# Performance work log

Hardware: AMD Instinct MI355X
Metric: run time of the kernel (lower is better)

The kernel has to match this reference:

```python
import jax, jax.numpy as jnp
import numpy as np

N = 100_000        # nodes
E = 3_200_000      # edges (avg degree 32)
H = 20             # hidden_channels (forced by forward body)
EH = 64            # edge_hidden_dim
EOUT = 10          # edge_output_dim (forced: 10 + EOUT == H)
THRESHOLD = 10.0


def setup_inputs() -> dict:
    key = jax.random.key(0)
    ks = jax.random.split(key, 12)
    x = jax.random.normal(ks[0], (N, 2, H), dtype=jnp.float32)
    edge_index = jax.random.randint(ks[1], (2, E), 0, N, dtype=jnp.int32)
    # distances must be in (0, threshold]
    edge_attr = jax.random.uniform(ks[2], (E, 1), dtype=jnp.float32, minval=1e-3, maxval=THRESHOLD)
    # module parameters (match torch init distributions: uniform[0,1))
    a = jax.random.uniform(ks[3], (1,), dtype=jnp.float32)
    b = jax.random.uniform(ks[4], (1,), dtype=jnp.float32) + 1.0
    gamma1 = jax.random.uniform(ks[5], (H, H), dtype=jnp.float32)
    gamma2 = jax.random.uniform(ks[6], (H, H), dtype=jnp.float32)
    bias = jax.random.uniform(ks[7], (H,), dtype=jnp.float32)
    # EdgeFeatureMLP2 params: Linear(1->EH), Linear(EH->EOUT)
    W1 = jax.random.normal(ks[8], (1, EH), dtype=jnp.float32)
    b1 = jax.random.normal(ks[9], (EH,), dtype=jnp.float32) * 0.1
    W2 = jax.random.normal(ks[10], (EH, EOUT), dtype=jnp.float32) / np.sqrt(EH)
    b2 = jax.random.normal(ks[11], (EOUT,), dtype=jnp.float32) * 0.1
    return dict(x=x, edge_index=edge_index, edge_attr=edge_attr, a=a, b=b,
                gamma1=gamma1, gamma2=gamma2, bias=bias, W1=W1, b1=b1, W2=W2, b2=b2)


def reference(x, edge_index, edge_attr, a, b, gamma1, gamma2, bias, W1, b1, W2, b2):
    src, dst = edge_index[0], edge_index[1]
    # edge MLP: Linear -> ReLU -> Linear -> ReLU
    h = jax.nn.relu(edge_attr @ W1 + b1)                    # [E, EH]
    mlp_out = jax.nn.relu(h @ W2 + b2)                      # [E, EOUT]
    # one-hot distance bucket: int(d / (threshold/10)), clipped to 9
    idx = jnp.minimum((edge_attr[:, 0] / (THRESHOLD / 10.0)).astype(jnp.int32), 9)
    one_hot = jax.nn.one_hot(idx, 10, dtype=edge_attr.dtype)  # [E, 10]
    comb = jnp.concatenate([one_hot, mlp_out], axis=1)      # [E, 20]
    # w_tilde: per-edge features normalized by the sum over all edges from the source node
    sum_w = jax.ops.segment_sum(comb, src, num_segments=N)  # [N, 20]
    sw = sum_w[src]                                         # [E, 20]
    nz = sw != 0
    w_tilde = jnp.where(nz, comb / jnp.where(nz, sw, 1.0), 0.01)
    # rho weighting: |a*h_j - (1-a)*h_j'|^b, elementwise over the 20-dim slot-0 features
    rho = jnp.abs(a * x[src, 0] - (1.0 - a) * x[dst, 0]) ** b  # [E, 20]
    sum_feat = jax.ops.segment_sum(rho * w_tilde, src, num_segments=N)  # [N, 20]
    # node update: relu(gamma1 @ x_j + gamma2 @ sum_feat_j + bias)
    out0 = jax.nn.relu(x[:, 0] @ gamma1.T + sum_feat @ gamma2.T + bias)  # [N, 20]
    return jnp.stack([out0, sum_feat], axis=1)              # [N, 2, 20]
```

## Files before the change

### kernel.cpp

```cpp
#include <hip/hip_runtime.h>

#define NN 100000
#define NE 3200000
#define HD 20
#define EHD 64
#define EOUTD 10
#define TBINS 4096

#define EPB 8192
#define NBLKS1 391
#define NBINS1 256
#define N1 (NBINS1 * NBLKS1)
#define NBUCK 196
#define WIN 4096
#define WPB 6
#define NWIN (NBUCK * WPB)
#define N2 (NBUCK * 512 * WPB)
#define KMASK 0x1FFFF

__global__ void scan1_kernel(int* __restrict__ data, int* __restrict__ bsum, int n) {
    __shared__ int s[1024];
    int t = threadIdx.x;
    int i = blockIdx.x * 1024 + t;
    int v = (i < n) ? data[i] : 0;
    s[t] = v;
    __syncthreads();
    for (int off = 1; off < 1024; off <<= 1) {
        int add = (t >= off) ? s[t - off] : 0;
        __syncthreads();
        s[t] += add;
        __syncthreads();
    }
    if (i < n) data[i] = s[t] - v;
    if (t == 1023) bsum[blockIdx.x] = s[t];
}

__global__ void scan3f_kernel(int* __restrict__ data, const int* __restrict__ bsum,
                              int nb, int n) {
    __shared__ int s[1024];
    int t = threadIdx.x;
    int v = (t < nb) ? bsum[t] : 0;
    s[t] = v;
    __syncthreads();
    for (int off = 1; off < 1024; off <<= 1) {
        int add = (t >= off) ? s[t - off] : 0;
        __syncthreads();
        s[t] += add;
        __syncthreads();
    }
    __syncthreads();
    int i = blockIdx.x * 1024 + t;
    if (i < n) data[i] += s[i >> 10] - ((i >> 10) < nb ? bsum[i >> 10] : 0);
}

__global__ void scan3bf_kernel(int* __restrict__ data, const int* __restrict__ bsum,
                               int nb, int* __restrict__ offsets) {
    __shared__ int s[1024];
    int t = threadIdx.x;
    int v = (t < nb) ? bsum[t] : 0;
    s[t] = v;
    __syncthreads();
    for (int off = 1; off < 1024; off <<= 1) {
        int add = (t >= off) ? s[t - off] : 0;
        __syncthreads();
        s[t] += add;
        __syncthreads();
    }
    __syncthreads();
    int i = blockIdx.x * 1024 + t;
    if (i >= N2) return;
    int blk = i >> 10;
    int vv = data[i] + s[blk] - (blk < nb ? bsum[blk] : 0);
    data[i] = vv;
    if (i % WPB == 0) {
        int nbidx = i / WPB;
        if (nbidx <= NN) offsets[nbidx] = vv;
    }
}

__global__ void hist1_kernel(const int* __restrict__ ei, int* __restrict__ counts1) {
    __shared__ int h[NBINS1];
    int t = threadIdx.x;
    if (t < NBINS1) h[t] = 0;
    __syncthreads();
    int base = blockIdx.x * EPB;
    for (int j = t; j < EPB; j += 1024) {
        int e = base + j;
        if (e < NE) atomicAdd(&h[ei[e] >> 9], 1);
    }
    __syncthreads();
    if (t < NBINS1) counts1[t * NBLKS1 + blockIdx.x] = h[t];
}

__global__ void scatter1_kernel(const int* __restrict__ ei,
                                const float* __restrict__ ea,
                                const int* __restrict__ counts1s,
                                int2* __restrict__ pk1) {
    __shared__ int cur[NBINS1];
    int t = threadIdx.x;
    if (t < NBINS1) cur[t] = counts1s[t * NBLKS1 + blockIdx.x];
    __syncthreads();
    int base = blockIdx.x * EPB;
    for (int j = t; j < EPB; j += 1024) {
        int e = base + j;
        if (e >= NE) break;
        int src = ei[e];
        int pos = atomicAdd(&cur[src >> 9], 1);
        int2 pk;
        pk.x = ei[NE + e] | ((src & 511) << 17);
        pk.y = __float_as_int(ea[e]);
        pk1[pos] = pk;
    }
}

__global__ void hist2_kernel(const int2* __restrict__ pk1,
                             const int* __restrict__ counts1s,
                             int* __restrict__ M2) {
    __shared__ int h[512];
    int t = threadIdx.x;
    h[t] = 0; h[t + 256] = 0;
    __syncthreads();
    int b = blockIdx.x / WPB, w = blockIdx.x % WPB;
    int bstart = counts1s[b * NBLKS1];
    int bend   = counts1s[(b + 1) * NBLKS1];
    int start = bstart + w * WIN;
    int end = (start + WIN < bend) ? (start + WIN) : bend;
    for (int i = start + t; i < end; i += 256)
        atomicAdd(&h[(pk1[i].x >> 17) & 511], 1);
    __syncthreads();
    M2[((b * 512) + t) * WPB + w]       = h[t];
    M2[((b * 512) + t + 256) * WPB + w] = h[t + 256];
}

__global__ void scatter2_kernel(const int2* __restrict__ pk1,
                                const int* __restrict__ counts1s,
                                const int* __restrict__ M2s,
                                int2* __restrict__ csr_pk) {
    __shared__ int cur[512];
    int t = threadIdx.x;
    int b = blockIdx.x / WPB, w = blockIdx.x % WPB;
    cur[t]       = M2s[((b * 512) + t) * WPB + w];
    cur[t + 256] = M2s[((b * 512) + t + 256) * WPB + w];
    __syncthreads();
    int bstart = counts1s[b * NBLKS1];
    int bend   = counts1s[(b + 1) * NBLKS1];
    int start = bstart + w * WIN;
    int end = (start + WIN < bend) ? (start + WIN) : bend;
    for (int i = start + t; i < end; i += 256) {
        int2 pk = pk1[i];
        int pos = atomicAdd(&cur[(pk.x >> 17) & 511], 1);
        pk.x &= KMASK;
        csr_pk[pos] = pk;
    }
}

__global__ void prep_kernel(const float* __restrict__ W1,
                            const float* __restrict__ b1,
                            const float* __restrict__ W2,
                            const float* __restrict__ b2,
                            const float* __restrict__ x,
                            unsigned short* __restrict__ tab,
                            int* __restrict__ xbf2) {
    const int TBLK = (TBINS + 255) / 256;
    if (blockIdx.x < TBLK) {
        int i = blockIdx.x * 256 + threadIdx.x;
        if (i >= TBINS) return;
        float m0[EOUTD], m1[EOUTD];
        float d0 = (float)i * (10.0f / (float)TBINS);
        float d1 = (float)(i + 1) * (10.0f / (float)TBINS);
        #pragma unroll
        for (int j = 0; j < EOUTD; ++j) { m0[j] = b2[j]; m1[j] = b2[j]; }
        for (int k = 0; k < EHD; ++k) {
            float h0 = fmaxf(fmaf(d0, W1[k], b1[k]), 0.0f);
            float h1 = fmaxf(fmaf(d1, W1[k], b1[k]), 0.0f);
            #pragma unroll
            for (int j = 0; j < EOUTD; ++j) {
                m0[j] = fmaf(h0, W2[k * EOUTD + j], m0[j]);
                m1[j] = fmaf(h1, W2[k * EOUTD + j], m1[j]);
            }
        }
        unsigned short* row = tab + (size_t)i * 32;
        #pragma unroll
        for (int j = 0; j < EOUTD; ++j) {
            unsigned int uv = __float_as_uint(m0[j]);
            unsigned int ud = __float_as_uint(m1[j] - m0[j]);
            uv = (uv + 0x7fffu + ((uv >> 16) & 1u)) >> 16;
            ud = (ud + 0x7fffu + ((ud >> 16) & 1u)) >> 16;
            row[2 * j]     = (unsigned short)uv;
            row[2 * j + 1] = (unsigned short)ud;
        }
        #pragma unroll
        for (int j = 20; j < 32; ++j) row[j] = 0;
    } else {
        int t = (blockIdx.x - TBLK) * 256 + threadIdx.x;
        if (t >= NN * 16) return;
        int node = t >> 4, k = t & 15;
        int v = 0;
        if (k < 10) {
            unsigned int u0 = __float_as_uint(x[(size_t)node * 2 * HD + k]);
            unsigned int u1 = __float_as_uint(x[(size_t)node * 2 * HD + k + 10]);
            u0 = (u0 + 0x7fffu + ((u0 >> 16) & 1u)) >> 16;
            u1 = (u1 + 0x7fffu + ((u1 >> 16) & 1u)) >> 16;
            v = (int)(u0 | (u1 << 16));
        }
        xbf2[t] = v;
    }
}

__launch_bounds__(256)
__global__ void node_kernel(const int* __restrict__ offsets,
                            const int2* __restrict__ csr_pk,
                            const float* __restrict__ x,
                            const int* __restrict__ xbf2,
                            const unsigned short* __restrict__ tab,
                            const float* __restrict__ pa,
                            const float* __restrict__ pb,
                            const float* __restrict__ g1,
                            const float* __restrict__ g2,
                            const float* __restrict__ bias,
                            float* __restrict__ out) {
    int tid  = threadIdx.x;
    int wave = tid >> 6;
    int lane = tid & 63;
    int sub  = lane / 10;
    int fk   = lane - sub * 10;
    int node = blockIdx.x * 24 + wave * 6 + sub;
    bool active = (sub < 6) && (node < NN);

    float a = pa[0], bb = pb[0];
    float oma = 1.0f - a;

    int off0 = 0, deg = 0;
    float xs_lo = 0.0f, xs_hi = 0.0f, axs_lo = 0.0f, axs_hi = 0.0f;
    if (active) {
        off0 = offsets[node];
        deg  = offsets[node + 1] - off0;
        xs_lo = x[(size_t)node * 2 * HD + fk];
        xs_hi = x[(size_t)node * 2 * HD + fk + 10];
        axs_lo = a * xs_lo;
        axs_hi = a * xs_hi;
    }

    float S0a = 0.0f, S1a = 0.0f, Sra = 0.0f;
    float S0b = 0.0f, S1b = 0.0f, Srb = 0.0f;

    auto process = [&](int dst, int db) {
        float d = __int_as_float(db);
        int idx = (int)d; if (idx > 9) idx = 9;
        float u = d * ((float)TBINS / 10.0f);
        int ti = (int)u; if (ti > TBINS - 1) ti = TBINS - 1;
        float fr = u - (float)ti;
        unsigned int xw = (unsigned int)xbf2[(((size_t)(unsigned int)dst) << 4) + fk];
        unsigned int tv = *(const unsigned int*)(tab + (((size_t)ti) << 5) + fk * 2);
        float xd_lo = __uint_as_float(xw << 16);
        float xd_hi = __uint_as_float(xw & 0xffff0000u);
        float t0 = fmaf(-oma, xd_lo, axs_lo);
        float t1 = fmaf(-oma, xd_hi, axs_hi);
        float r0 = (t0 != 0.0f)
            ? __builtin_amdgcn_exp2f(bb * __builtin_amdgcn_logf(fabsf(t0))) : 0.0f;
        float r1 = (t1 != 0.0f)
            ? __builtin_amdgcn_exp2f(bb * __builtin_amdgcn_logf(fabsf(t1))) : 0.0f;
        Sra += r0; Srb += r1;
        float c0 = (fk == idx) ? 1.0f : 0.0f;
        float val = __uint_as_float(tv << 16);
        float del = __uint_as_float(tv & 0xffff0000u);
        float c1 = fmaxf(fmaf(fr, del, val), 0.0f);
        S0a += c0; S1a = fmaf(r0, c0, S1a);
        S0b += c1; S1b = fmaf(r1, c1, S1b);
    };

    for (int base = 0; base < deg; base += 10) {
        int nchunk = deg - base; if (nchunk > 10) nchunk = 10;
        int idxc = off0 + base + ((fk < nchunk) ? fk : (nchunk - 1));
        int2 pk = csr_pk[idxc];
        int dstv = pk.x, dbits = pk.y;
        int jj = 0;
        for (; jj + 1 < nchunk; jj += 2) {
            int dA = __shfl(dstv, sub * 10 + jj, 64);
            int bA = __shfl(dbits, sub * 10 + jj, 64);
            int dB = __shfl(dstv, sub * 10 + jj + 1, 64);
            int bB = __shfl(dbits, sub * 10 + jj + 1, 64);
            process(dA, bA);
            process(dB, bB);
        }
        if (jj < nchunk) {
            int dA = __shfl(dstv, sub * 10 + jj, 64);
            int bA = __shfl(dbits, sub * 10 + jj, 64);
            process(dA, bA);
        }
    }

    float sf_lo = (S0a != 0.0f) ? (S1a / S0a) : (0.01f * Sra);
    float sf_hi = (S0b != 0.0f) ? (S1b / S0b) : (0.01f * Srb);

    if (active) {
        float acc0 = bias[fk];
        float acc1 = bias[fk + 10];
        const float* g1r0 = g1 + fk * HD;
        const float* g1r1 = g1 + (fk + 10) * HD;
        const float* g2r0 = g2 + fk * HD;
        const float* g2r1 = g2 + (fk + 10) * HD;
        #pragma unroll
        for (int j = 0; j < 10; ++j) {
            int sl = sub * 10 + j;
            float xj  = __shfl(xs_lo, sl, 64);
            float xj1 = __shfl(xs_hi, sl, 64);
            float sj  = __shfl(sf_lo, sl, 64);
            float sj1 = __shfl(sf_hi, sl, 64);
            acc0 = fmaf(xj, g1r0[j], acc0);  acc0 = fmaf(xj1, g1r0[j + 10], acc0);
            acc0 = fmaf(sj, g2r0[j], acc0);  acc0 = fmaf(sj1, g2r0[j + 10], acc0);
            acc1 = fmaf(xj, g1r1[j], acc1);  acc1 = fmaf(xj1, g1r1[j + 10], acc1);
            acc1 = fmaf(sj, g2r1[j], acc1);  acc1 = fmaf(sj1, g2r1[j + 10], acc1);
        }
        float* op = out + (size_t)node * 2 * HD;
        op[fk]          = fmaxf(acc0, 0.0f);
        op[fk + 10]     = fmaxf(acc1, 0.0f);
        op[HD + fk]     = sf_lo;
        op[HD + fk + 10] = sf_hi;
    }
}

extern "C" void kernel_launch(void* const* d_in, const int* in_sizes, int n_in,
                              void* d_out, int out_size, void* d_ws, size_t ws_size,
                              hipStream_t stream) {
    const float* x    = (const float*)d_in[0];
    const int*   ei   = (const int*)d_in[1];
    const float* ea   = (const float*)d_in[2];
    const float* pa   = (const float*)d_in[3];
    const float* pb   = (const float*)d_in[4];
    const float* g1   = (const float*)d_in[5];
    const float* g2   = (const float*)d_in[6];
    const float* bias = (const float*)d_in[7];
    const float* W1   = (const float*)d_in[8];
    const float* b1   = (const float*)d_in[9];
    const float* W2   = (const float*)d_in[10];
    const float* b2   = (const float*)d_in[11];
    float* out = (float*)d_out;

    char* ws = (char*)d_ws;
    int*   counts1 = (int*)ws;     ws += ((size_t)N1 * 4 + 127) / 128 * 128;
    int*   bsum1   = (int*)ws;     ws += (1024 * 4 + 127) / 128 * 128;
    int*   M2      = (int*)ws;     ws += ((size_t)N2 * 4 + 127) / 128 * 128;
    int*   bsum2   = (int*)ws;     ws += (1024 * 4 + 127) / 128 * 128;
    int*   offsets = (int*)ws;     ws += ((size_t)(NN + 1) * 4 + 127) / 128 * 128;
    int2*  pk1     = (int2*)ws;    ws += (size_t)NE * 8;
    int2*  csr_pk  = (int2*)ws;    ws += (size_t)NE * 8;
    unsigned short* tab = (unsigned short*)ws;   ws += ((size_t)TBINS * 32 * 2 + 127) / 128 * 128;
    int*   xbf2    = (int*)ws;     ws += ((size_t)NN * 16 * 4 + 127) / 128 * 128;

    const int TBLK = (TBINS + 255) / 256;
    prep_kernel<<<TBLK + (NN * 16 + 255) / 256, 256, 0, stream>>>(W1, b1, W2, b2, x,
                                                                  tab, xbf2);

    const int nb1 = (N1 + 1023) / 1024;
    hist1_kernel<<<NBLKS1, 1024, 0, stream>>>(ei, counts1);
    scan1_kernel<<<nb1, 1024, 0, stream>>>(counts1, bsum1, N1);
    scan3f_kernel<<<nb1, 1024, 0, stream>>>(counts1, bsum1, nb1, N1);
    scatter1_kernel<<<NBLKS1, 1024, 0, stream>>>(ei, ea, counts1, pk1);

    const int nb2 = (N2 + 1023) / 1024;
    hist2_kernel<<<NWIN, 256, 0, stream>>>(pk1, counts1, M2);
    scan1_kernel<<<nb2, 1024, 0, stream>>>(M2, bsum2, N2);
    scan3bf_kernel<<<nb2, 1024, 0, stream>>>(M2, bsum2, nb2, offsets);
    scatter2_kernel<<<NWIN, 256, 0, stream>>>(pk1, counts1, M2, csr_pk);

    node_kernel<<<(NN + 23) / 24, 256, 0, stream>>>(offsets, csr_pk, x, xbf2, tab,
                                                    pa, pb, g1, g2, bias, out);
}
```

Baseline: 174.6 us.

## Pack 4 features per lane, 5-lane node groups, precompute bin indices in scatter

```diff
diff --git a/kernel.cpp b/kernel.cpp
--- a/kernel.cpp
+++ b/kernel.cpp
@@ -149,7 +149,14 @@
     for (int i = start + t; i < end; i += 256) {
         int2 pk = pk1[i];
         int pos = atomicAdd(&cur[(pk.x >> 17) & 511], 1);
+        float d = __int_as_float(pk.y);
+        int idx = (int)d; if (idx > 9) idx = 9;
+        float u = d * ((float)TBINS / 10.0f);
+        int ti = (int)u; if (ti > TBINS - 1) ti = TBINS - 1;
+        float fr = u - (float)ti;
+        int fr16 = (int)(fr * 65536.0f); if (fr16 > 65535) fr16 = 65535;
         pk.x &= KMASK;
+        pk.y = fr16 | (ti << 16) | (idx << 28);
         csr_pk[pos] = pk;
     }
 }
@@ -159,9 +166,13 @@
                             const float* __restrict__ W2,
                             const float* __restrict__ b2,
                             const float* __restrict__ x,
-                            unsigned short* __restrict__ tab,
-                            int* __restrict__ xbf2) {
+                            int2* __restrict__ tab2,
+                            int2* __restrict__ xbf4) {
     const int TBLK = (TBINS + 255) / 256;
+    auto bf16 = [](float f) -> unsigned int {
+        unsigned int u = __float_as_uint(f);
+        return (u + 0x7fffu + ((u >> 16) & 1u)) >> 16;
+    };
     if (blockIdx.x < TBLK) {
         int i = blockIdx.x * 256 + threadIdx.x;
         if (i >= TBINS) return;
@@ -179,31 +190,23 @@
                 m1[j] = fmaf(h1, W2[k * EOUTD + j], m1[j]);
             }
         }
-        unsigned short* row = tab + (size_t)i * 32;
         #pragma unroll
-        for (int j = 0; j < EOUTD; ++j) {
-            unsigned int uv = __float_as_uint(m0[j]);
-            unsigned int ud = __float_as_uint(m1[j] - m0[j]);
-            uv = (uv + 0x7fffu + ((uv >> 16) & 1u)) >> 16;
-            ud = (ud + 0x7fffu + ((ud >> 16) & 1u)) >> 16;
-            row[2 * j]     = (unsigned short)uv;
-            row[2 * j + 1] = (unsigned short)ud;
+        for (int p = 0; p < 5; ++p) {
+            int2 tv;
+            tv.x = (int)(bf16(m0[p]) | (bf16(m1[p] - m0[p]) << 16));
+            tv.y = (int)(bf16(m0[p + 5]) | (bf16(m1[p + 5] - m0[p + 5]) << 16));
+            tab2[(size_t)i * 5 + p] = tv;
         }
-        #pragma unroll
-        for (int j = 20; j < 32; ++j) row[j] = 0;
     } else {
         int t = (blockIdx.x - TBLK) * 256 + threadIdx.x;
-        if (t >= NN * 16) return;
-        int node = t >> 4, k = t & 15;
-        int v = 0;
-        if (k < 10) {
-            unsigned int u0 = __float_as_uint(x[(size_t)node * 2 * HD + k]);
-            unsigned int u1 = __float_as_uint(x[(size_t)node * 2 * HD + k + 10]);
-            u0 = (u0 + 0x7fffu + ((u0 >> 16) & 1u)) >> 16;
-            u1 = (u1 + 0x7fffu + ((u1 >> 16) & 1u)) >> 16;
-            v = (int)(u0 | (u1 << 16));
-        }
-        xbf2[t] = v;
+        if (t >= NN * 5) return;
+        int node = t / 5;
+        int p = t - node * 5;
+        const float* xp = x + (size_t)node * 2 * HD;
+        int2 v;
+        v.x = (int)(bf16(xp[p]) | (bf16(xp[p + 5]) << 16));
+        v.y = (int)(bf16(xp[p + 10]) | (bf16(xp[p + 15]) << 16));
+        xbf4[t] = v;
     }
 }
 
@@ -211,8 +214,8 @@
 __global__ void node_kernel(const int* __restrict__ offsets,
                             const int2* __restrict__ csr_pk,
                             const float* __restrict__ x,
-                            const int* __restrict__ xbf2,
-                            const unsigned short* __restrict__ tab,
+                            const int2* __restrict__ xbf4,
+                            const int2* __restrict__ tab2,
                             const float* __restrict__ pa,
                             const float* __restrict__ pb,
                             const float* __restrict__ g1,
@@ -222,101 +225,132 @@
     int tid  = threadIdx.x;
     int wave = tid >> 6;
     int lane = tid & 63;
-    int sub  = lane / 10;
-    int fk   = lane - sub * 10;
-    int node = blockIdx.x * 24 + wave * 6 + sub;
-    bool active = (sub < 6) && (node < NN);
+    int sub  = lane / 5;
+    int fk   = lane - sub * 5;
+    int node = blockIdx.x * 48 + wave * 12 + sub;
+    bool active = (sub < 12) && (node < NN);
 
     float a = pa[0], bb = pb[0];
     float oma = 1.0f - a;
 
     int off0 = 0, deg = 0;
-    float xs_lo = 0.0f, xs_hi = 0.0f, axs_lo = 0.0f, axs_hi = 0.0f;
+    float xs0 = 0.0f, xs1 = 0.0f, xs2 = 0.0f, xs3 = 0.0f;
     if (active) {
         off0 = offsets[node];
         deg  = offsets[node + 1] - off0;
-        xs_lo = x[(size_t)node * 2 * HD + fk];
-        xs_hi = x[(size_t)node * 2 * HD + fk + 10];
-        axs_lo = a * xs_lo;
-        axs_hi = a * xs_hi;
-    }
-
-    float S0a = 0.0f, S1a = 0.0f, Sra = 0.0f;
-    float S0b = 0.0f, S1b = 0.0f, Srb = 0.0f;
-
-    auto process = [&](int dst, int db) {
-        float d = __int_as_float(db);
-        int idx = (int)d; if (idx > 9) idx = 9;
-        float u = d * ((float)TBINS / 10.0f);
-        int ti = (int)u; if (ti > TBINS - 1) ti = TBINS - 1;
-        float fr = u - (float)ti;
-        unsigned int xw = (unsigned int)xbf2[(((size_t)(unsigned int)dst) << 4) + fk];
-        unsigned int tv = *(const unsigned int*)(tab + (((size_t)ti) << 5) + fk * 2);
-        float xd_lo = __uint_as_float(xw << 16);
-        float xd_hi = __uint_as_float(xw & 0xffff0000u);
-        float t0 = fmaf(-oma, xd_lo, axs_lo);
-        float t1 = fmaf(-oma, xd_hi, axs_hi);
+        const float* xp = x + (size_t)node * 2 * HD;
+        xs0 = xp[fk]; xs1 = xp[fk + 5]; xs2 = xp[fk + 10]; xs3 = xp[fk + 15];
+    }
+    float ax0 = a * xs0, ax1 = a * xs1, ax2 = a * xs2, ax3 = a * xs3;
+
+    float S00 = 0.0f, S10 = 0.0f, Sr0 = 0.0f;
+    float S01 = 0.0f, S11 = 0.0f, Sr1 = 0.0f;
+    float S02 = 0.0f, S12 = 0.0f, Sr2 = 0.0f;
+    float S03 = 0.0f, S13 = 0.0f, Sr3 = 0.0f;
+
+    auto process = [&](int dst, int dy) {
+        int ti  = (dy >> 16) & 0xFFF;
+        int idx = (dy >> 28) & 0xF;
+        float fr = (float)(dy & 0xFFFF) * (1.0f / 65536.0f);
+        int2 xw = xbf4[(size_t)(unsigned int)dst * 5 + fk];
+        int2 tv = tab2[(size_t)ti * 5 + fk];
+        float xd0 = __uint_as_float(((unsigned int)xw.x) << 16);
+        float xd1 = __uint_as_float(((unsigned int)xw.x) & 0xffff0000u);
+        float xd2 = __uint_as_float(((unsigned int)xw.y) << 16);
+        float xd3 = __uint_as_float(((unsigned int)xw.y) & 0xffff0000u);
+        float t0 = fmaf(-oma, xd0, ax0);
+        float t1 = fmaf(-oma, xd1, ax1);
+        float t2 = fmaf(-oma, xd2, ax2);
+        float t3 = fmaf(-oma, xd3, ax3);
         float r0 = (t0 != 0.0f)
             ? __builtin_amdgcn_exp2f(bb * __builtin_amdgcn_logf(fabsf(t0))) : 0.0f;
         float r1 = (t1 != 0.0f)
             ? __builtin_amdgcn_exp2f(bb * __builtin_amdgcn_logf(fabsf(t1))) : 0.0f;
-        Sra += r0; Srb += r1;
-        float c0 = (fk == idx) ? 1.0f : 0.0f;
-        float val = __uint_as_float(tv << 16);
-        float del = __uint_as_float(tv & 0xffff0000u);
-        float c1 = fmaxf(fmaf(fr, del, val), 0.0f);
-        S0a += c0; S1a = fmaf(r0, c0, S1a);
-        S0b += c1; S1b = fmaf(r1, c1, S1b);
+        float r2 = (t2 != 0.0f)
+            ? __builtin_amdgcn_exp2f(bb * __builtin_amdgcn_logf(fabsf(t2))) : 0.0f;
+        float r3 = (t3 != 0.0f)
+            ? __builtin_amdgcn_exp2f(bb * __builtin_amdgcn_logf(fabsf(t3))) : 0.0f;
+        Sr0 += r0; Sr1 += r1; Sr2 += r2; Sr3 += r3;
+        float c0 = (idx == fk) ? 1.0f : 0.0f;
+        float c1 = (idx == fk + 5) ? 1.0f : 0.0f;
+        float va = __uint_as_float(((unsigned int)tv.x) << 16);
+        float da = __uint_as_float(((unsigned int)tv.x) & 0xffff0000u);
+        float vb = __uint_as_float(((unsigned int)tv.y) << 16);
+        float db2 = __uint_as_float(((unsigned int)tv.y) & 0xffff0000u);
+        float c2 = fmaxf(fmaf(fr, da, va), 0.0f);
+        float c3 = fmaxf(fmaf(fr, db2, vb), 0.0f);
+        S00 += c0; S10 = fmaf(r0, c0, S10);
+        S01 += c1; S11 = fmaf(r1, c1, S11);
+        S02 += c2; S12 = fmaf(r2, c2, S12);
+        S03 += c3; S13 = fmaf(r3, c3, S13);
     };
 
-    for (int base = 0; base < deg; base += 10) {
-        int nchunk = deg - base; if (nchunk > 10) nchunk = 10;
+    for (int base = 0; base < deg; base += 5) {
+        int nchunk = deg - base; if (nchunk > 5) nchunk = 5;
         int idxc = off0 + base + ((fk < nchunk) ? fk : (nchunk - 1));
         int2 pk = csr_pk[idxc];
         int dstv = pk.x, dbits = pk.y;
         int jj = 0;
         for (; jj + 1 < nchunk; jj += 2) {
-            int dA = __shfl(dstv, sub * 10 + jj, 64);
-            int bA = __shfl(dbits, sub * 10 + jj, 64);
-            int dB = __shfl(dstv, sub * 10 + jj + 1, 64);
-            int bB = __shfl(dbits, sub * 10 + jj + 1, 64);
+            int dA = __shfl(dstv, sub * 5 + jj, 64);
+            int bA = __shfl(dbits, sub * 5 + jj, 64);
+            int dB = __shfl(dstv, sub * 5 + jj + 1, 64);
+            int bB = __shfl(dbits, sub * 5 + jj + 1, 64);
             process(dA, bA);
             process(dB, bB);
         }
         if (jj < nchunk) {
-            int dA = __shfl(dstv, sub * 10 + jj, 64);
-            int bA = __shfl(dbits, sub * 10 + jj, 64);
+            int dA = __shfl(dstv, sub * 5 + jj, 64);
+            int bA = __shfl(dbits, sub * 5 + jj, 64);
             process(dA, bA);
         }
     }
 
-    float sf_lo = (S0a != 0.0f) ? (S1a / S0a) : (0.01f * Sra);
-    float sf_hi = (S0b != 0.0f) ? (S1b / S0b) : (0.01f * Srb);
+    float sf0 = (S00 != 0.0f) ? (S10 / S00) : (0.01f * Sr0);
+    float sf1 = (S01 != 0.0f) ? (S11 / S01) : (0.01f * Sr1);
+    float sf2 = (S02 != 0.0f) ? (S12 / S02) : (0.01f * Sr2);
+    float sf3 = (S03 != 0.0f) ? (S13 / S03) : (0.01f * Sr3);
 
     if (active) {
-        float acc0 = bias[fk];
-        float acc1 = bias[fk + 10];
-        const float* g1r0 = g1 + fk * HD;
-        const float* g1r1 = g1 + (fk + 10) * HD;
-        const float* g2r0 = g2 + fk * HD;
-        const float* g2r1 = g2 + (fk + 10) * HD;
+        int r0 = fk, r1 = fk + 5, r2 = fk + 10, r3 = fk + 15;
+        float a0 = bias[r0], a1 = bias[r1], a2 = bias[r2], a3 = bias[r3];
+        const float* g10 = g1 + r0 * HD; const float* g20 = g2 + r0 * HD;
+        const float* g11 = g1 + r1 * HD; const float* g21 = g2 + r1 * HD;
+        const float* g12 = g1 + r2 * HD; const float* g22 = g2 + r2 * HD;
+        const float* g13 = g1 + r3 * HD; const float* g23 = g2 + r3 * HD;
         #pragma unroll
-        for (int j = 0; j < 10; ++j) {
-            int sl = sub * 10 + j;
-            float xj  = __shfl(xs_lo, sl, 64);
-            float xj1 = __shfl(xs_hi, sl, 64);
-            float sj  = __shfl(sf_lo, sl, 64);
-            float sj1 = __shfl(sf_hi, sl, 64);
-            acc0 = fmaf(xj, g1r0[j], acc0);  acc0 = fmaf(xj1, g1r0[j + 10], acc0);
-            acc0 = fmaf(sj, g2r0[j], acc0);  acc0 = fmaf(sj1, g2r0[j + 10], acc0);
-            acc1 = fmaf(xj, g1r1[j], acc1);  acc1 = fmaf(xj1, g1r1[j + 10], acc1);
-            acc1 = fmaf(sj, g2r1[j], acc1);  acc1 = fmaf(sj1, g2r1[j + 10], acc1);
+        for (int j = 0; j < 5; ++j) {
+            int sl = sub * 5 + j;
+            float xa = __shfl(xs0, sl, 64), xb = __shfl(xs1, sl, 64);
+            float xc = __shfl(xs2, sl, 64), xd = __shfl(xs3, sl, 64);
+            float sa = __shfl(sf0, sl, 64), sb = __shfl(sf1, sl, 64);
+            float sc = __shfl(sf2, sl, 64), sd = __shfl(sf3, sl, 64);
+            a0 = fmaf(xa, g10[j], a0); a0 = fmaf(xb, g10[j + 5], a0);
+            a0 = fmaf(xc, g10[j + 10], a0); a0 = fmaf(xd, g10[j + 15], a0);
+            a0 = fmaf(sa, g20[j], a0); a0 = fmaf(sb, g20[j + 5], a0);
+            a0 = fmaf(sc, g20[j + 10], a0); a0 = fmaf(sd, g20[j + 15], a0);
+            a1 = fmaf(xa, g11[j], a1); a1 = fmaf(xb, g11[j + 5], a1);
+            a1 = fmaf(xc, g11[j + 10], a1); a1 = fmaf(xd, g11[j + 15], a1);
+            a1 = fmaf(sa, g21[j], a1); a1 = fmaf(sb, g21[j + 5], a1);
+            a1 = fmaf(sc, g21[j + 10], a1); a1 = fmaf(sd, g21[j + 15], a1);
+            a2 = fmaf(xa, g12[j], a2); a2 = fmaf(xb, g12[j + 5], a2);
+            a2 = fmaf(xc, g12[j + 10], a2); a2 = fmaf(xd, g12[j + 15], a2);
+            a2 = fmaf(sa, g22[j], a2); a2 = fmaf(sb, g22[j + 5], a2);
+            a2 = fmaf(sc, g22[j + 10], a2); a2 = fmaf(sd, g22[j + 15], a2);
+            a3 = fmaf(xa, g13[j], a3); a3 = fmaf(xb, g13[j + 5], a3);
+            a3 = fmaf(xc, g13[j + 10], a3); a3 = fmaf(xd, g13[j + 15], a3);
+            a3 = fmaf(sa, g23[j], a3); a3 = fmaf(sb, g23[j + 5], a3);
+            a3 = fmaf(sc, g23[j + 10], a3); a3 = fmaf(sd, g23[j + 15], a3);
         }
         float* op = out + (size_t)node * 2 * HD;
-        op[fk]          = fmaxf(acc0, 0.0f);
-        op[fk + 10]     = fmaxf(acc1, 0.0f);
-        op[HD + fk]     = sf_lo;
-        op[HD + fk + 10] = sf_hi;
+        op[r0] = fmaxf(a0, 0.0f);
+        op[r1] = fmaxf(a1, 0.0f);
+        op[r2] = fmaxf(a2, 0.0f);
+        op[r3] = fmaxf(a3, 0.0f);
+        op[HD + r0] = sf0;
+        op[HD + r1] = sf1;
+        op[HD + r2] = sf2;
+        op[HD + r3] = sf3;
     }
 }
 
@@ -345,12 +379,12 @@
     int*   offsets = (int*)ws;     ws += ((size_t)(NN + 1) * 4 + 127) / 128 * 128;
     int2*  pk1     = (int2*)ws;    ws += (size_t)NE * 8;
     int2*  csr_pk  = (int2*)ws;    ws += (size_t)NE * 8;
-    unsigned short* tab = (unsigned short*)ws;   ws += ((size_t)TBINS * 32 * 2 + 127) / 128 * 128;
-    int*   xbf2    = (int*)ws;     ws += ((size_t)NN * 16 * 4 + 127) / 128 * 128;
+    int2*  tab2    = (int2*)ws;    ws += ((size_t)TBINS * 5 * 8 + 127) / 128 * 128;
+    int2*  xbf4    = (int2*)ws;    ws += ((size_t)NN * 5 * 8 + 127) / 128 * 128;
 
     const int TBLK = (TBINS + 255) / 256;
-    prep_kernel<<<TBLK + (NN * 16 + 255) / 256, 256, 0, stream>>>(W1, b1, W2, b2, x,
-                                                                  tab, xbf2);
+    prep_kernel<<<TBLK + (NN * 5 + 255) / 256, 256, 0, stream>>>(W1, b1, W2, b2, x,
+                                                                 tab2, xbf4);
 
     const int nb1 = (N1 + 1023) / 1024;
     hist1_kernel<<<NBLKS1, 1024, 0, stream>>>(ei, counts1);
@@ -364,6 +398,6 @@
     scan3bf_kernel<<<nb2, 1024, 0, stream>>>(M2, bsum2, nb2, offsets);
     scatter2_kernel<<<NWIN, 256, 0, stream>>>(pk1, counts1, M2, csr_pk);
 
-    node_kernel<<<(NN + 23) / 24, 256, 0, stream>>>(offsets, csr_pk, x, xbf2, tab,
+    node_kernel<<<(NN + 47) / 48, 256, 0, stream>>>(offsets, csr_pk, x, xbf4, tab2,
                                                     pa, pb, g1, g2, bias, out);
 }
```

Result: slower. 216.1 us (+23.7%).
